# Performance work log

Hardware: AMD Instinct MI355X
Metric: run time of the kernel (lower is better)

Reference implementation:

```python
import jax, jax.numpy as jnp
import numpy as np

NUM_NODES = 500000
DIM = 128
BATCH = 131072
MOMENTUM = 0.9


def setup_inputs() -> dict:
    key = jax.random.key(0)
    ks = jax.random.split(key, 6)
    s = 1.0 / np.sqrt(DIM)
    return {
        "hidden": jax.random.normal(ks[0], (NUM_NODES, DIM), jnp.float32),
        "variance": jnp.ones((NUM_NODES, DIM), jnp.float32),
        "idx": jnp.arange(BATCH, dtype=jnp.int64 if jax.config.jax_enable_x64 else jnp.int32),
        "new_repr": jax.random.normal(ks[1], (BATCH, DIM), jnp.float32),
        "W_ih": jax.random.normal(ks[2], (3 * DIM, DIM), jnp.float32) * s,
        "W_hh": jax.random.normal(ks[3], (3 * DIM, DIM), jnp.float32) * s,
        "b_ih": jax.random.normal(ks[4], (3 * DIM,), jnp.float32) * s,
        "b_hh": jax.random.normal(ks[5], (3 * DIM,), jnp.float32) * s,
    }


def _gru_cell(x, h, W_ih, W_hh, b_ih, b_hh):
    # torch GRUCell gate layout: [reset | update | new], each of size DIM
    gi = x @ W_ih.T + b_ih          # [B, 3*DIM]
    gh = h @ W_hh.T + b_hh          # [B, 3*DIM]
    gi_r, gi_z, gi_n = jnp.split(gi, 3, axis=-1)
    gh_r, gh_z, gh_n = jnp.split(gh, 3, axis=-1)
    r = jax.nn.sigmoid(gi_r + gh_r)
    z = jax.nn.sigmoid(gi_z + gh_z)
    n = jnp.tanh(gi_n + r * gh_n)
    return (1.0 - z) * n + z * h


def reference(hidden, variance, idx, new_repr, W_ih, W_hh, b_ih, b_hh):
    h_prev = hidden[idx]                                   # gather [B, DIM]
    h_new = _gru_cell(new_repr, h_prev, W_ih, W_hh, b_ih, b_hh)
    delta = h_new - h_prev
    var_new = MOMENTUM * variance[idx] + (1.0 - MOMENTUM) * delta * delta
    hidden_out = hidden.at[idx].set(h_new)                 # scatter write
    variance_out = variance.at[idx].set(var_new)
    return jnp.stack([hidden_out, variance_out])           # [2, N, DIM]
```

## Files before the change

### kernel.cpp

```cpp
#include <hip/hip_runtime.h>
#include <hip/hip_bf16.h>
#include <cstdint>
#include <cstddef>

#define NUM_NODES 500000
#define DIM 128
#define BATCH 131072

typedef __attribute__((ext_vector_type(8))) short short8;
typedef __attribute__((ext_vector_type(4))) short short4_t;
typedef __attribute__((ext_vector_type(4))) float f32x4;

static __device__ __forceinline__ short f2bf(float f) {
    unsigned u = __builtin_bit_cast(unsigned, f);
    u += 0x7fffu + ((u >> 16) & 1u);
    return (short)(u >> 16);
}

__global__ void k_init(unsigned char* __restrict__ mask,
                       const float* __restrict__ Wih,
                       const float* __restrict__ Whh,
                       short* __restrict__ WbIH,
                       short* __restrict__ WbHH,
                       int do_mask) {
    int i = blockIdx.x * blockDim.x + threadIdx.x;
    if (do_mask && i < NUM_NODES) mask[i] = 0;
    if (i < 3 * DIM * DIM) {
        WbIH[i] = f2bf(Wih[i]);
        WbHH[i] = f2bf(Whh[i]);
    }
}

__global__ void k_scatter(unsigned char* __restrict__ mask, const int* __restrict__ idx) {
    int i = blockIdx.x * blockDim.x + threadIdx.x;
    if (i < BATCH) mask[idx[i]] = 1;
}

__global__ void __launch_bounds__(256)
k_copy(const float* __restrict__ hidden,
       const float* __restrict__ variance,
       const unsigned char* __restrict__ mask,
       float* __restrict__ out0,
       float* __restrict__ out1) {
    int gid = blockIdx.x * 256 + threadIdx.x;
    int row = gid >> 4;
    int c8  = gid & 15;
    if (mask && mask[row]) return;
    size_t off = (size_t)row * DIM + c8 * 8;
    f32x4 a0 = *(const f32x4*)(hidden + off);
    f32x4 a1 = *(const f32x4*)(hidden + off + 4);
    f32x4 b0 = *(const f32x4*)(variance + off);
    f32x4 b1 = *(const f32x4*)(variance + off + 4);
    *(f32x4*)(out0 + off)     = a0;
    *(f32x4*)(out0 + off + 4) = a1;
    *(f32x4*)(out1 + off)     = b0;
    *(f32x4*)(out1 + off + 4) = b1;
}

__global__ void __launch_bounds__(512)
k_gru(const float* __restrict__ hidden,
      const float* __restrict__ variance,
      const int*   __restrict__ idx,
      const float* __restrict__ xg,
      const short* __restrict__ WbIH,
      const short* __restrict__ WbHH,
      const float* __restrict__ b_ih,
      const float* __restrict__ b_hh,
      float* __restrict__ out0,
      float* __restrict__ out1) {
    __shared__ __align__(16) char smem[34304];
    short (*Xb)[136] = (short(*)[136])smem;
    short (*Hb)[136] = (short(*)[136])(smem + 8704);
    float (*Hf)[132] = (float(*)[132])(smem + 17408);
    float (*Hn)[132] = (float(*)[132])smem;

    const int t  = threadIdx.x;
    const int rb = blockIdx.x * 32;

    for (int j = t; j < 1024; j += 512) {
        int row = j >> 5, c4 = j & 31;
        int node = idx[rb + row];
        f32x4 xv = *(const f32x4*)(xg + (size_t)(rb + row) * DIM + c4 * 4);
        f32x4 hv = *(const f32x4*)(hidden + (size_t)node * DIM + c4 * 4);
        short4_t xs, hs;
        xs.x = f2bf(xv.x); xs.y = f2bf(xv.y); xs.z = f2bf(xv.z); xs.w = f2bf(xv.w);
        hs.x = f2bf(hv.x); hs.y = f2bf(hv.y); hs.z = f2bf(hv.z); hs.w = f2bf(hv.w);
        *(short4_t*)&Xb[row][c4 * 4] = xs;
        *(short4_t*)&Hb[row][c4 * 4] = hs;
        *(f32x4*)&Hf[row][c4 * 4]    = hv;
    }
    __syncthreads();

    const int w  = t >> 6;
    const int l  = t & 63;
    const int c  = l & 15;
    const int gq = l >> 4;

    f32x4 acc[2][3][2] = {};

    #pragma unroll
    for (int ks = 0; ks < 4; ++ks) {
        const int k0 = ks * 32 + gq * 8;
        short8 a[2][2];
        a[0][0] = *(const short8*)&Xb[c][k0];
        a[1][0] = *(const short8*)&Xb[16 + c][k0];
        a[0][1] = *(const short8*)&Hb[c][k0];
        a[1][1] = *(const short8*)&Hb[16 + c][k0];
        #pragma unroll
        for (int th = 0; th < 3; ++th) {
            const int o = w * 16 + th * 128 + c;
            const short8 bi = *(const short8*)(WbIH + (size_t)o * DIM + k0);
            const short8 bh = *(const short8*)(WbHH + (size_t)o * DIM + k0);
            #pragma unroll
            for (int mt = 0; mt < 2; ++mt) {
                acc[mt][th][0] = __builtin_amdgcn_mfma_f32_16x16x32_bf16(a[mt][0], bi, acc[mt][th][0], 0, 0, 0);
                acc[mt][th][1] = __builtin_amdgcn_mfma_f32_16x16x32_bf16(a[mt][1], bh, acc[mt][th][1], 0, 0, 0);
            }
        }
    }

    __syncthreads();

    const int d = w * 16 + c;
    const float bs_r = b_ih[d]       + b_hh[d];
    const float bs_z = b_ih[d + 128] + b_hh[d + 128];
    const float bi_n = b_ih[d + 256];
    const float bh_n = b_hh[d + 256];

    #pragma unroll
    for (int mt = 0; mt < 2; ++mt) {
        #pragma unroll
        for (int r = 0; r < 4; ++r) {
            const int m = mt * 16 + gq * 4 + r;
            float s_r  = acc[mt][0][0][r] + acc[mt][0][1][r] + bs_r;
            float s_z  = acc[mt][1][0][r] + acc[mt][1][1][r] + bs_z;
            float gi_n = acc[mt][2][0][r] + bi_n;
            float gh_n = acc[mt][2][1][r] + bh_n;
            float rg = 1.f / (1.f + __expf(-s_r));
            float zg = 1.f / (1.f + __expf(-s_z));
            float aa = gi_n + rg * gh_n;
            float n  = 1.f - 2.f / (__expf(2.f * aa) + 1.f);
            float h  = Hf[m][d];
            Hn[m][d] = (1.f - zg) * n + zg * h;
        }
    }
    __syncthreads();

    for (int j = t; j < 1024; j += 512) {
        int row = j >> 5, c4 = j & 31;
        int node = idx[rb + row];
        size_t off = (size_t)node * DIM + c4 * 4;
        f32x4 hn = *(f32x4*)&Hn[row][c4 * 4];
        f32x4 h  = *(f32x4*)&Hf[row][c4 * 4];
        f32x4 vv = *(const f32x4*)(variance + off);
        f32x4 var;
        var.x = 0.9f * vv.x + 0.1f * (hn.x - h.x) * (hn.x - h.x);
        var.y = 0.9f * vv.y + 0.1f * (hn.y - h.y) * (hn.y - h.y);
        var.z = 0.9f * vv.z + 0.1f * (hn.z - h.z) * (hn.z - h.z);
        var.w = 0.9f * vv.w + 0.1f * (hn.w - h.w) * (hn.w - h.w);
        *(f32x4*)(out0 + off) = hn;
        *(f32x4*)(out1 + off) = var;
    }
}

extern "C" void kernel_launch(void* const* d_in, const int* in_sizes, int n_in,
                              void* d_out, int out_size, void* d_ws, size_t ws_size,
                              hipStream_t stream) {
    const float* hidden   = (const float*)d_in[0];
    const float* variance = (const float*)d_in[1];
    const int*   idx      = (const int*)d_in[2];
    const float* x        = (const float*)d_in[3];
    const float* Wih      = (const float*)d_in[4];
    const float* Whh      = (const float*)d_in[5];
    const float* bih      = (const float*)d_in[6];
    const float* bhh      = (const float*)d_in[7];
    float* out0 = (float*)d_out;
    float* out1 = out0 + (size_t)NUM_NODES * DIM;

    const size_t maskBytes = (size_t)NUM_NODES;
    const size_t wBytes    = (size_t)3 * DIM * DIM * 2;
    const bool   have_mask = ws_size >= maskBytes + 16 + 2 * wBytes;

    unsigned char* mask = have_mask ? (unsigned char*)d_ws : nullptr;
    short* WbIH = have_mask ? (short*)((char*)d_ws + ((maskBytes + 15) & ~size_t(15)))
                            : (short*)d_ws;
    short* WbHH = WbIH + 3 * DIM * DIM;

    k_init<<<(NUM_NODES + 255) / 256, 256, 0, stream>>>(
        mask ? mask : (unsigned char*)d_ws, Wih, Whh, WbIH, WbHH, have_mask ? 1 : 0);

    if (have_mask)
        k_scatter<<<BATCH / 256, 256, 0, stream>>>(mask, idx);

    k_copy<<<(NUM_NODES * 16) / 256, 256, 0, stream>>>(
        hidden, variance, mask, out0, out1);

    k_gru<<<BATCH / 32, 512, 0, stream>>>(hidden, variance, idx, x,
                                          WbIH, WbHH, bih, bhh, out0, out1);
}
```

Baseline: 293.2 us.

## Move variance update out of GRU kernel into a full-table finalize pass

The GRU kernel now keeps only the bf16 copies of x and h in shared memory and writes h_new straight to the scattered output rows. It drops the fp32 staging, the Hn write-back and the variance epilogue. A new finalize kernel streams over every row: for rows flagged in the mask it rebuilds the variance from hidden, variance and out0, and for all other rows it copies. The aim is to shrink shared memory and syncs in the GRU kernel and move the variance read/update into a coalesced streaming pass. In exchange the batch rows of hidden and out0 are read a second time, the GRU stores become scalar, and the GRU blend now uses the bf16-rounded h rather than fp32.

```diff
diff --git a/kernel.cpp b/kernel.cpp
--- a/kernel.cpp
+++ b/kernel.cpp
@@ -15,6 +15,10 @@
     unsigned u = __builtin_bit_cast(unsigned, f);
     u += 0x7fffu + ((u >> 16) & 1u);
     return (short)(u >> 16);
+}
+static __device__ __forceinline__ float bf2f(short s) {
+    unsigned u = ((unsigned)(unsigned short)s) << 16;
+    return __builtin_bit_cast(float, u);
 }
 
 __global__ void k_init(unsigned char* __restrict__ mask,
@@ -36,48 +40,24 @@
     if (i < BATCH) mask[idx[i]] = 1;
 }
 
-__global__ void __launch_bounds__(256)
-k_copy(const float* __restrict__ hidden,
-       const float* __restrict__ variance,
-       const unsigned char* __restrict__ mask,
-       float* __restrict__ out0,
-       float* __restrict__ out1) {
-    int gid = blockIdx.x * 256 + threadIdx.x;
-    int row = gid >> 4;
-    int c8  = gid & 15;
-    if (mask && mask[row]) return;
-    size_t off = (size_t)row * DIM + c8 * 8;
-    f32x4 a0 = *(const f32x4*)(hidden + off);
-    f32x4 a1 = *(const f32x4*)(hidden + off + 4);
-    f32x4 b0 = *(const f32x4*)(variance + off);
-    f32x4 b1 = *(const f32x4*)(variance + off + 4);
-    *(f32x4*)(out0 + off)     = a0;
-    *(f32x4*)(out0 + off + 4) = a1;
-    *(f32x4*)(out1 + off)     = b0;
-    *(f32x4*)(out1 + off + 4) = b1;
-}
-
 __global__ void __launch_bounds__(512)
 k_gru(const float* __restrict__ hidden,
-      const float* __restrict__ variance,
       const int*   __restrict__ idx,
       const float* __restrict__ xg,
       const short* __restrict__ WbIH,
       const short* __restrict__ WbHH,
       const float* __restrict__ b_ih,
       const float* __restrict__ b_hh,
-      float* __restrict__ out0,
-      float* __restrict__ out1) {
-    __shared__ __align__(16) char smem[34304];
-    short (*Xb)[136] = (short(*)[136])smem;
-    short (*Hb)[136] = (short(*)[136])(smem + 8704);
-    float (*Hf)[132] = (float(*)[132])(smem + 17408);
-    float (*Hn)[132] = (float(*)[132])smem;
+      float* __restrict__ out0) {
+    __shared__ __align__(16) short Xb[32][136];
+    __shared__ __align__(16) short Hb[32][136];
 
     const int t  = threadIdx.x;
     const int rb = blockIdx.x * 32;
 
-    for (int j = t; j < 1024; j += 512) {
+    #pragma unroll
+    for (int jj = 0; jj < 2; ++jj) {
+        int j = t + jj * 512;
         int row = j >> 5, c4 = j & 31;
         int node = idx[rb + row];
         f32x4 xv = *(const f32x4*)(xg + (size_t)(rb + row) * DIM + c4 * 4);
@@ -87,7 +67,6 @@
         hs.x = f2bf(hv.x); hs.y = f2bf(hv.y); hs.z = f2bf(hv.z); hs.w = f2bf(hv.w);
         *(short4_t*)&Xb[row][c4 * 4] = xs;
         *(short4_t*)&Hb[row][c4 * 4] = hs;
-        *(f32x4*)&Hf[row][c4 * 4]    = hv;
     }
     __syncthreads();
 
@@ -119,8 +98,6 @@
         }
     }
 
-    __syncthreads();
-
     const int d = w * 16 + c;
     const float bs_r = b_ih[d]       + b_hh[d];
     const float bs_z = b_ih[d + 128] + b_hh[d + 128];
@@ -140,27 +117,99 @@
             float zg = 1.f / (1.f + __expf(-s_z));
             float aa = gi_n + rg * gh_n;
             float n  = 1.f - 2.f / (__expf(2.f * aa) + 1.f);
-            float h  = Hf[m][d];
-            Hn[m][d] = (1.f - zg) * n + zg * h;
+            float h  = bf2f(Hb[m][d]);
+            float hn = (1.f - zg) * n + zg * h;
+            int node = idx[rb + m];
+            out0[(size_t)node * DIM + d] = hn;
         }
     }
-    __syncthreads();
-
-    for (int j = t; j < 1024; j += 512) {
-        int row = j >> 5, c4 = j & 31;
-        int node = idx[rb + row];
-        size_t off = (size_t)node * DIM + c4 * 4;
-        f32x4 hn = *(f32x4*)&Hn[row][c4 * 4];
-        f32x4 h  = *(f32x4*)&Hf[row][c4 * 4];
-        f32x4 vv = *(const f32x4*)(variance + off);
-        f32x4 var;
-        var.x = 0.9f * vv.x + 0.1f * (hn.x - h.x) * (hn.x - h.x);
-        var.y = 0.9f * vv.y + 0.1f * (hn.y - h.y) * (hn.y - h.y);
-        var.z = 0.9f * vv.z + 0.1f * (hn.z - h.z) * (hn.z - h.z);
-        var.w = 0.9f * vv.w + 0.1f * (hn.w - h.w) * (hn.w - h.w);
-        *(f32x4*)(out0 + off) = hn;
-        *(f32x4*)(out1 + off) = var;
-    }
+}
+
+__global__ void __launch_bounds__(256)
+k_fin(const float* __restrict__ hidden,
+      const float* __restrict__ variance,
+      const unsigned char* __restrict__ mask,
+      float* __restrict__ out0,
+      float* __restrict__ out1) {
+    int gid = blockIdx.x * 256 + threadIdx.x;
+    int row = gid >> 4;
+    int c8  = gid & 15;
+    size_t off = (size_t)row * DIM + c8 * 8;
+    f32x4 h0 = *(const f32x4*)(hidden + off);
+    f32x4 h1 = *(const f32x4*)(hidden + off + 4);
+    f32x4 v0 = *(const f32x4*)(variance + off);
+    f32x4 v1 = *(const f32x4*)(variance + off + 4);
+    if (mask[row]) {
+        f32x4 n0 = *(const f32x4*)(out0 + off);
+        f32x4 n1 = *(const f32x4*)(out0 + off + 4);
+        f32x4 w0, w1;
+        float d;
+        d = n0.x - h0.x; w0.x = 0.9f * v0.x + 0.1f * d * d;
+        d = n0.y - h0.y; w0.y = 0.9f * v0.y + 0.1f * d * d;
+        d = n0.z - h0.z; w0.z = 0.9f * v0.z + 0.1f * d * d;
+        d = n0.w - h0.w; w0.w = 0.9f * v0.w + 0.1f * d * d;
+        d = n1.x - h1.x; w1.x = 0.9f * v1.x + 0.1f * d * d;
+        d = n1.y - h1.y; w1.y = 0.9f * v1.y + 0.1f * d * d;
+        d = n1.z - h1.z; w1.z = 0.9f * v1.z + 0.1f * d * d;
+        d = n1.w - h1.w; w1.w = 0.9f * v1.w + 0.1f * d * d;
+        *(f32x4*)(out1 + off)     = w0;
+        *(f32x4*)(out1 + off + 4) = w1;
+    } else {
+        *(f32x4*)(out0 + off)     = h0;
+        *(f32x4*)(out0 + off + 4) = h1;
+        *(f32x4*)(out1 + off)     = v0;
+        *(f32x4*)(out1 + off + 4) = v1;
+    }
+}
+
+__global__ void __launch_bounds__(256)
+k_varfix(const float* __restrict__ hidden,
+         const float* __restrict__ variance,
+         const int* __restrict__ idx,
+         const float* __restrict__ out0,
+         float* __restrict__ out1) {
+    int gid = blockIdx.x * 256 + threadIdx.x;
+    int i   = gid >> 4;
+    int c8  = gid & 15;
+    int node = idx[i];
+    size_t off = (size_t)node * DIM + c8 * 8;
+    f32x4 h0 = *(const f32x4*)(hidden + off);
+    f32x4 h1 = *(const f32x4*)(hidden + off + 4);
+    f32x4 v0 = *(const f32x4*)(variance + off);
+    f32x4 v1 = *(const f32x4*)(variance + off + 4);
+    f32x4 n0 = *(const f32x4*)(out0 + off);
+    f32x4 n1 = *(const f32x4*)(out0 + off + 4);
+    f32x4 w0, w1;
+    float d;
+    d = n0.x - h0.x; w0.x = 0.9f * v0.x + 0.1f * d * d;
+    d = n0.y - h0.y; w0.y = 0.9f * v0.y + 0.1f * d * d;
+    d = n0.z - h0.z; w0.z = 0.9f * v0.z + 0.1f * d * d;
+    d = n0.w - h0.w; w0.w = 0.9f * v0.w + 0.1f * d * d;
+    d = n1.x - h1.x; w1.x = 0.9f * v1.x + 0.1f * d * d;
+    d = n1.y - h1.y; w1.y = 0.9f * v1.y + 0.1f * d * d;
+    d = n1.z - h1.z; w1.z = 0.9f * v1.z + 0.1f * d * d;
+    d = n1.w - h1.w; w1.w = 0.9f * v1.w + 0.1f * d * d;
+    *(f32x4*)(out1 + off)     = w0;
+    *(f32x4*)(out1 + off + 4) = w1;
+}
+
+__global__ void __launch_bounds__(256)
+k_copyall(const float* __restrict__ hidden,
+          const float* __restrict__ variance,
+          float* __restrict__ out0,
+          float* __restrict__ out1) {
+    int gid = blockIdx.x * 256 + threadIdx.x;
+    int row = gid >> 4;
+    int c8  = gid & 15;
+    size_t off = (size_t)row * DIM + c8 * 8;
+    f32x4 a0 = *(const f32x4*)(hidden + off);
+    f32x4 a1 = *(const f32x4*)(hidden + off + 4);
+    f32x4 b0 = *(const f32x4*)(variance + off);
+    f32x4 b1 = *(const f32x4*)(variance + off + 4);
+    *(f32x4*)(out0 + off)     = a0;
+    *(f32x4*)(out0 + off + 4) = a1;
+    *(f32x4*)(out1 + off)     = b0;
+    *(f32x4*)(out1 + off + 4) = b1;
 }
 
 extern "C" void kernel_launch(void* const* d_in, const int* in_sizes, int n_in,
@@ -189,12 +238,18 @@
     k_init<<<(NUM_NODES + 255) / 256, 256, 0, stream>>>(
         mask ? mask : (unsigned char*)d_ws, Wih, Whh, WbIH, WbHH, have_mask ? 1 : 0);
 
-    if (have_mask)
+    if (have_mask) {
         k_scatter<<<BATCH / 256, 256, 0, stream>>>(mask, idx);
-
-    k_copy<<<(NUM_NODES * 16) / 256, 256, 0, stream>>>(
-        hidden, variance, mask, out0, out1);
-
-    k_gru<<<BATCH / 32, 512, 0, stream>>>(hidden, variance, idx, x,
-                                          WbIH, WbHH, bih, bhh, out0, out1);
-}
+        k_gru<<<BATCH / 32, 512, 0, stream>>>(hidden, idx, x,
+                                              WbIH, WbHH, bih, bhh, out0);
+        k_fin<<<(NUM_NODES * 16) / 256, 256, 0, stream>>>(
+            hidden, variance, mask, out0, out1);
+    } else {
+        k_copyall<<<(NUM_NODES * 16) / 256, 256, 0, stream>>>(
+            hidden, variance, out0, out1);
+        k_gru<<<BATCH / 32, 512, 0, stream>>>(hidden, idx, x,
+                                              WbIH, WbHH, bih, bhh, out0);
+        k_varfix<<<(BATCH * 16) / 256, 256, 0, stream>>>(
+            hidden, variance, idx, out0, out1);
+    }
+}
```

Measured after the change: 293.6 us. No clear change (+0.2%).

## Load GRU MFMA operands directly from global memory and drop LDS staging

Applied to the files above, without the earlier changes.

The GRU kernel no longer stages the x and h tiles through shared memory. Each wave now loads and converts its MFMA A-operands straight from global memory, and the epilogue reads h and variance per element and writes the outputs as scalar stores. This removes the LDS traffic and three barriers. In exchange, all 8 waves now redundantly read the same x and h rows from global or L2, and the output stores become strided 4-byte accesses instead of coalesced 16-byte vectors.

```diff
diff --git a/kernel.cpp b/kernel.cpp
--- a/kernel.cpp
+++ b/kernel.cpp
@@ -8,13 +8,21 @@
 #define BATCH 131072
 
 typedef __attribute__((ext_vector_type(8))) short short8;
-typedef __attribute__((ext_vector_type(4))) short short4_t;
 typedef __attribute__((ext_vector_type(4))) float f32x4;
 
 static __device__ __forceinline__ short f2bf(float f) {
     unsigned u = __builtin_bit_cast(unsigned, f);
     u += 0x7fffu + ((u >> 16) & 1u);
     return (short)(u >> 16);
+}
+
+static __device__ __forceinline__ short8 cvt8(const float* __restrict__ p) {
+    f32x4 a = *(const f32x4*)p;
+    f32x4 b = *(const f32x4*)(p + 4);
+    short8 s;
+    s[0] = f2bf(a.x); s[1] = f2bf(a.y); s[2] = f2bf(a.z); s[3] = f2bf(a.w);
+    s[4] = f2bf(b.x); s[5] = f2bf(b.y); s[6] = f2bf(b.z); s[7] = f2bf(b.w);
+    return s;
 }
 
 __global__ void k_init(unsigned char* __restrict__ mask,
@@ -68,58 +76,40 @@
       const float* __restrict__ b_hh,
       float* __restrict__ out0,
       float* __restrict__ out1) {
-    __shared__ __align__(16) char smem[34304];
-    short (*Xb)[136] = (short(*)[136])smem;
-    short (*Hb)[136] = (short(*)[136])(smem + 8704);
-    float (*Hf)[132] = (float(*)[132])(smem + 17408);
-    float (*Hn)[132] = (float(*)[132])smem;
-
     const int t  = threadIdx.x;
-    const int rb = blockIdx.x * 32;
-
-    for (int j = t; j < 1024; j += 512) {
-        int row = j >> 5, c4 = j & 31;
-        int node = idx[rb + row];
-        f32x4 xv = *(const f32x4*)(xg + (size_t)(rb + row) * DIM + c4 * 4);
-        f32x4 hv = *(const f32x4*)(hidden + (size_t)node * DIM + c4 * 4);
-        short4_t xs, hs;
-        xs.x = f2bf(xv.x); xs.y = f2bf(xv.y); xs.z = f2bf(xv.z); xs.w = f2bf(xv.w);
-        hs.x = f2bf(hv.x); hs.y = f2bf(hv.y); hs.z = f2bf(hv.z); hs.w = f2bf(hv.w);
-        *(short4_t*)&Xb[row][c4 * 4] = xs;
-        *(short4_t*)&Hb[row][c4 * 4] = hs;
-        *(f32x4*)&Hf[row][c4 * 4]    = hv;
-    }
-    __syncthreads();
-
     const int w  = t >> 6;
     const int l  = t & 63;
     const int c  = l & 15;
     const int gq = l >> 4;
+    const int rb = blockIdx.x * 32;
+
+    const int r0 = rb + c, r1 = rb + 16 + c;
+    const int n0 = idx[r0], n1 = idx[r1];
+    const float* xp0 = xg + (size_t)r0 * DIM;
+    const float* xp1 = xg + (size_t)r1 * DIM;
+    const float* hp0 = hidden + (size_t)n0 * DIM;
+    const float* hp1 = hidden + (size_t)n1 * DIM;
 
     f32x4 acc[2][3][2] = {};
 
     #pragma unroll
     for (int ks = 0; ks < 4; ++ks) {
         const int k0 = ks * 32 + gq * 8;
-        short8 a[2][2];
-        a[0][0] = *(const short8*)&Xb[c][k0];
-        a[1][0] = *(const short8*)&Xb[16 + c][k0];
-        a[0][1] = *(const short8*)&Hb[c][k0];
-        a[1][1] = *(const short8*)&Hb[16 + c][k0];
+        const short8 aX0 = cvt8(xp0 + k0);
+        const short8 aX1 = cvt8(xp1 + k0);
+        const short8 aH0 = cvt8(hp0 + k0);
+        const short8 aH1 = cvt8(hp1 + k0);
         #pragma unroll
         for (int th = 0; th < 3; ++th) {
             const int o = w * 16 + th * 128 + c;
             const short8 bi = *(const short8*)(WbIH + (size_t)o * DIM + k0);
             const short8 bh = *(const short8*)(WbHH + (size_t)o * DIM + k0);
-            #pragma unroll
-            for (int mt = 0; mt < 2; ++mt) {
-                acc[mt][th][0] = __builtin_amdgcn_mfma_f32_16x16x32_bf16(a[mt][0], bi, acc[mt][th][0], 0, 0, 0);
-                acc[mt][th][1] = __builtin_amdgcn_mfma_f32_16x16x32_bf16(a[mt][1], bh, acc[mt][th][1], 0, 0, 0);
-            }
+            acc[0][th][0] = __builtin_amdgcn_mfma_f32_16x16x32_bf16(aX0, bi, acc[0][th][0], 0, 0, 0);
+            acc[1][th][0] = __builtin_amdgcn_mfma_f32_16x16x32_bf16(aX1, bi, acc[1][th][0], 0, 0, 0);
+            acc[0][th][1] = __builtin_amdgcn_mfma_f32_16x16x32_bf16(aH0, bh, acc[0][th][1], 0, 0, 0);
+            acc[1][th][1] = __builtin_amdgcn_mfma_f32_16x16x32_bf16(aH1, bh, acc[1][th][1], 0, 0, 0);
         }
     }
-
-    __syncthreads();
 
     const int d = w * 16 + c;
     const float bs_r = b_ih[d]       + b_hh[d];
@@ -140,26 +130,14 @@
             float zg = 1.f / (1.f + __expf(-s_z));
             float aa = gi_n + rg * gh_n;
             float n  = 1.f - 2.f / (__expf(2.f * aa) + 1.f);
-            float h  = Hf[m][d];
-            Hn[m][d] = (1.f - zg) * n + zg * h;
+            int node = idx[rb + m];
+            size_t off = (size_t)node * DIM + d;
+            float h  = hidden[off];
+            float hn = (1.f - zg) * n + zg * h;
+            float dl = hn - h;
+            out0[off] = hn;
+            out1[off] = 0.9f * variance[off] + 0.1f * dl * dl;
         }
-    }
-    __syncthreads();
-
-    for (int j = t; j < 1024; j += 512) {
-        int row = j >> 5, c4 = j & 31;
-        int node = idx[rb + row];
-        size_t off = (size_t)node * DIM + c4 * 4;
-        f32x4 hn = *(f32x4*)&Hn[row][c4 * 4];
-        f32x4 h  = *(f32x4*)&Hf[row][c4 * 4];
-        f32x4 vv = *(const f32x4*)(variance + off);
-        f32x4 var;
-        var.x = 0.9f * vv.x + 0.1f * (hn.x - h.x) * (hn.x - h.x);
-        var.y = 0.9f * vv.y + 0.1f * (hn.y - h.y) * (hn.y - h.y);
-        var.z = 0.9f * vv.z + 0.1f * (hn.z - h.z) * (hn.z - h.z);
-        var.w = 0.9f * vv.w + 0.1f * (hn.w - h.w) * (hn.w - h.w);
-        *(f32x4*)(out0 + off) = hn;
-        *(f32x4*)(out1 + off) = var;
     }
 }
 
```

New measurement: 390.6 us. 33.2% more time.
